# Kernel optimization log

Measured on AMD Instinct MI355X. Metric: run time of the kernel, lower is better.

Reference implementation:

```python
import jax, jax.numpy as jnp
import numpy as np

D_MODEL = 1024
NUM_HEADS = 16
HEAD_DIM = D_MODEL // NUM_HEADS


def setup_inputs() -> dict:
    key = jax.random.key(0)
    ks = jax.random.split(key, 5)
    scale = 1.0 / np.sqrt(D_MODEL)
    x = jax.random.normal(ks[0], (2, 2048, D_MODEL), dtype=jnp.float32)
    W_qkv = jax.random.normal(ks[1], (D_MODEL, 3 * D_MODEL), dtype=jnp.float32) * scale
    b_qkv = jnp.zeros((3 * D_MODEL,), dtype=jnp.float32)
    W_proj = jax.random.normal(ks[2], (D_MODEL, D_MODEL), dtype=jnp.float32) * scale
    b_proj = jnp.zeros((D_MODEL,), dtype=jnp.float32)
    return {"x": x, "W_qkv": W_qkv, "b_qkv": b_qkv, "W_proj": W_proj, "b_proj": b_proj}


def reference(x, W_qkv, b_qkv, W_proj, b_proj):
    B, S, D = x.shape
    qkv = x @ W_qkv + b_qkv                      # [B,S,3D]
    qkv = qkv.reshape(B, S, 3, NUM_HEADS, HEAD_DIM)
    qkv = jnp.transpose(qkv, (2, 0, 3, 1, 4))    # [3,B,H,S,hd]
    q, k, v = qkv[0], qkv[1], qkv[2]
    scores = jnp.einsum('bhqd,bhkd->bhqk', q, k) / jnp.sqrt(jnp.asarray(HEAD_DIM, x.dtype))
    probs = jax.nn.softmax(scores, axis=-1)
    out = jnp.einsum('bhqk,bhkd->bhqd', probs, v)  # [B,H,S,hd]
    out = jnp.transpose(out, (0, 2, 1, 3)).reshape(B, S, D)
    return out @ W_proj + b_proj
```

## Files before the change

### kernel.cpp

```cpp
#include <hip/hip_runtime.h>
#include <math.h>

#define B_ 2
#define S_ 2048
#define D_ 1024
#define H_ 16
#define HD_ 64

typedef __bf16 bf16x8 __attribute__((ext_vector_type(8)));
typedef __bf16 bf16x4 __attribute__((ext_vector_type(4)));
typedef __bf16 bf16x2 __attribute__((ext_vector_type(2)));
typedef float f32x4 __attribute__((ext_vector_type(4)));
typedef float f32x16 __attribute__((ext_vector_type(16)));
typedef unsigned u32x2 __attribute__((ext_vector_type(2)));

#define GLOAD16(gsrc, ldst) \
  __builtin_amdgcn_global_load_lds((const __attribute__((address_space(1))) void*)(gsrc), \
                                   (__attribute__((address_space(3))) void*)(ldst), 16, 0, 0)

#define QSCALE 0.18033688f

static __device__ __forceinline__ unsigned pack2(float a, float b) {
    bf16x2 v; v[0] = (__bf16)a; v[1] = (__bf16)b;
    return __builtin_bit_cast(unsigned, v);
}

__global__ __launch_bounds__(256) void prep_k(
    const float* __restrict__ x, __bf16* __restrict__ x_bf,
    const float* __restrict__ Wqkv, __bf16* __restrict__ wq_t,
    const float* __restrict__ Wproj, __bf16* __restrict__ wp_t)
{
    __shared__ float t[64][65];
    const int tid = threadIdx.x;
    const int bid = blockIdx.x;

    if (bid < 2048) {
        int i = (bid * 256 + tid) * 8;
        float4 a = *(const float4*)(x + i);
        float4 b = *(const float4*)(x + i + 4);
        bf16x8 v;
        v[0] = (__bf16)a.x; v[1] = (__bf16)a.y; v[2] = (__bf16)a.z; v[3] = (__bf16)a.w;
        v[4] = (__bf16)b.x; v[5] = (__bf16)b.y; v[6] = (__bf16)b.z; v[7] = (__bf16)b.w;
        *(bf16x8*)(x_bf + i) = v;
        return;
    }

    const float* in; __bf16* outp; int K, N, qcols; float qs; int bx, by;
    if (bid < 2816) {
        int tt = bid - 2048; bx = tt % 48; by = tt / 48;
        in = Wqkv; outp = wq_t; K = D_; N = 3 * D_; qcols = D_; qs = QSCALE;
    } else {
        int tt = bid - 2816; bx = tt % 16; by = tt / 16;
        in = Wproj; outp = wp_t; K = D_; N = D_; qcols = 0; qs = 1.0f;
    }
    const int bj = bx * 64;
    const int bi = by * 64;
    #pragma unroll
    for (int it = 0; it < 4; ++it) {
        int idx = (tid + it * 256) * 4;
        int r = idx >> 6, c = idx & 63;
        float4 v = *(const float4*)(in + (size_t)(bi + r) * N + bj + c);
        t[r][c] = v.x; t[r][c+1] = v.y; t[r][c+2] = v.z; t[r][c+3] = v.w;
    }
    __syncthreads();
    int j = tid & 63;
    int i0 = (tid >> 6) * 16;
    float s = (bj + j) < qcols ? qs : 1.0f;
    bf16x8 h0, h1;
    #pragma unroll
    for (int ii = 0; ii < 8; ++ii) h0[ii] = (__bf16)(t[i0 + ii][j] * s);
    #pragma unroll
    for (int ii = 0; ii < 8; ++ii) h1[ii] = (__bf16)(t[i0 + 8 + ii][j] * s);
    size_t o = (size_t)(bj + j) * K + bi + i0;
    *(bf16x8*)(outp + o) = h0; *(bf16x8*)(outp + o + 8) = h1;
}

__global__ __launch_bounds__(256) void gemm_nt_k(
    const __bf16* __restrict__ A, const __bf16* __restrict__ Bt,
    const float* __restrict__ bias, __bf16* __restrict__ C,
    int M, int N, int K, int qcols, float qs)
{
    constexpr int TSZ = 128 * 64;
    __shared__ __bf16 sA[TSZ];
    __shared__ __bf16 sB[TSZ];

    const int tid = threadIdx.x, w = tid >> 6, l = tid & 63;
    const int lr = l & 15, lg = l >> 4;
    const int bm = blockIdx.y * 128, bn = blockIdx.x * 128;
    const int wm = w >> 1, wn = w & 1;

    f32x4 acc[4][4] = {};

    for (int k0 = 0; k0 < K; k0 += 64) {
        __syncthreads();
        #pragma unroll
        for (int c = 0; c < 4; ++c) {
            int q = w * 4 + c;
            int r = q * 8 + (l >> 3);
            int sl = ((l & 7) ^ (r & 7)) * 8;
            GLOAD16(A + (size_t)(bm + r) * K + k0 + sl, sA + q * 512);
            GLOAD16(Bt + (size_t)(bn + r) * K + k0 + sl, sB + q * 512);
        }
        __syncthreads();
        #pragma unroll
        for (int kk = 0; kk < 2; ++kk) {
            bf16x8 ah[4], bh[4];
            #pragma unroll
            for (int i = 0; i < 4; ++i) {
                int ra = wm * 64 + i * 16 + lr;
                int sa = ((kk * 4 + lg) ^ (ra & 7)) * 8;
                ah[i] = *(const bf16x8*)(sA + ra * 64 + sa);
                int rb = wn * 64 + i * 16 + lr;
                int sb = ((kk * 4 + lg) ^ (rb & 7)) * 8;
                bh[i] = *(const bf16x8*)(sB + rb * 64 + sb);
            }
            #pragma unroll
            for (int mi = 0; mi < 4; ++mi)
                #pragma unroll
                for (int ni = 0; ni < 4; ++ni)
                    acc[mi][ni] = __builtin_amdgcn_mfma_f32_16x16x32_bf16(ah[mi], bh[ni], acc[mi][ni], 0, 0, 0);
        }
    }

    #pragma unroll
    for (int ni = 0; ni < 4; ++ni) {
        int col = bn + wn * 64 + ni * 16 + lr;
        float bv = bias[col];
        if (col < qcols) bv *= qs;
        #pragma unroll
        for (int mi = 0; mi < 4; ++mi) {
            #pragma unroll
            for (int r = 0; r < 4; ++r) {
                int row = bm + wm * 64 + mi * 16 + lg * 4 + r;
                float v = acc[mi][ni][r] + bv;
                C[(size_t)row * N + col] = (__bf16)v;
            }
        }
    }
}

__global__ __launch_bounds__(256) void gemm2_comb_k(
    const __bf16* __restrict__ P, const float* __restrict__ L,
    const __bf16* __restrict__ Bt, const float* __restrict__ bias,
    float* __restrict__ C)
{
    constexpr int K = D_, N = D_;
    constexpr size_t PS = (size_t)4096 * 1024;
    constexpr int LS = 4096 * 16;
    constexpr int TSZ = 128 * 64;
    __shared__ __bf16 sA[TSZ];
    __shared__ __bf16 sB[TSZ];

    const int tid = threadIdx.x, w = tid >> 6, l = tid & 63;
    const int lr = l & 15, lg = l >> 4;
    const int bm = blockIdx.y * 128, bn = blockIdx.x * 128;
    const int wm = w >> 1, wn = w & 1;

    int arow[4], asl[4];
    #pragma unroll
    for (int c = 0; c < 4; ++c) {
        int q = w * 4 + c;
        int r = q * 8 + (l >> 3);
        arow[c] = r;
        asl[c] = ((l & 7) ^ (r & 7)) * 8;
    }

    f32x4 acc[4][4] = {};

    for (int k0 = 0; k0 < K; k0 += 64) {
        const int h = k0 >> 6;
        __syncthreads();
        #pragma unroll
        for (int c = 0; c < 4; ++c) {
            int q = w * 4 + c;
            int sl = asl[c];
            GLOAD16(Bt + (size_t)(bn + arow[c]) * K + k0 + sl, sB + q * 512);
            size_t off = (size_t)(bm + arow[c]) * D_ + k0 + sl;
            bf16x8 p0 = *(const bf16x8*)(P + off);
            bf16x8 p1 = *(const bf16x8*)(P + PS + off);
            float inv = 1.0f / (L[(bm + arow[c]) * 16 + h] + L[LS + (bm + arow[c]) * 16 + h]);
            bf16x8 a;
            #pragma unroll
            for (int j = 0; j < 8; ++j)
                a[j] = (__bf16)(((float)p0[j] + (float)p1[j]) * inv);
            *(bf16x8*)(sA + q * 512 + l * 8) = a;
        }
        __syncthreads();
        #pragma unroll
        for (int kk = 0; kk < 2; ++kk) {
            bf16x8 ah[4], bh[4];
            #pragma unroll
            for (int i = 0; i < 4; ++i) {
                int ra = wm * 64 + i * 16 + lr;
                int sa = ((kk * 4 + lg) ^ (ra & 7)) * 8;
                ah[i] = *(const bf16x8*)(sA + ra * 64 + sa);
                int rb = wn * 64 + i * 16 + lr;
                int sb = ((kk * 4 + lg) ^ (rb & 7)) * 8;
                bh[i] = *(const bf16x8*)(sB + rb * 64 + sb);
            }
            #pragma unroll
            for (int mi = 0; mi < 4; ++mi)
                #pragma unroll
                for (int ni = 0; ni < 4; ++ni)
                    acc[mi][ni] = __builtin_amdgcn_mfma_f32_16x16x32_bf16(ah[mi], bh[ni], acc[mi][ni], 0, 0, 0);
        }
    }

    #pragma unroll
    for (int ni = 0; ni < 4; ++ni) {
        int col = bn + wn * 64 + ni * 16 + lr;
        float bv = bias[col];
        #pragma unroll
        for (int mi = 0; mi < 4; ++mi) {
            #pragma unroll
            for (int r = 0; r < 4; ++r) {
                int row = bm + wm * 64 + mi * 16 + lg * 4 + r;
                C[(size_t)row * N + col] = acc[mi][ni][r] + bv;
            }
        }
    }
}

__global__ __launch_bounds__(256, 2) void attn32_k(
    const __bf16* __restrict__ qkv, __bf16* __restrict__ Pout,
    float* __restrict__ Lout)
{
    __shared__ __bf16 Ks[2][64 * 64];
    __shared__ __bf16 Vt[2][64 * 64];

    const int tid = threadIdx.x, w = tid >> 6, l = tid & 63;
    const int q32 = l & 31, hi = l >> 5;
    const int bid = blockIdx.x;
    const int X = bid >> 5, hb = bid & 31;
    const int qt = X >> 1, kvh = X & 1;
    const int h = hb >> 1, b = hb & 1;
    const int q0 = qt * 256;
    const int kvbase = kvh * 1024;
    const size_t ldq = 3 * D_;
    const __bf16* Qg = qkv + (size_t)b * S_ * ldq + h * HD_;
    const __bf16* Kg = Qg + D_;
    const __bf16* Vg = Qg + 2 * D_;
    const int qg0 = q0 + w * 64 + q32;

    bf16x8 qf0[4], qf1[4];
    #pragma unroll
    for (int ds = 0; ds < 4; ++ds) {
        qf0[ds] = *(const bf16x8*)(Qg + (size_t)qg0 * ldq + ds * 16 + hi * 8);
        qf1[ds] = *(const bf16x8*)(Qg + (size_t)(qg0 + 32) * ldq + ds * 16 + hi * 8);
    }

    int krow[2], ksl[2], voff[2][8];
    const int vk = l;
    #pragma unroll
    for (int c = 0; c < 2; ++c) {
        int p = (w * 2 + c) * 64 + l;
        krow[c] = p >> 3;
        ksl[c]  = (p & 7) ^ (krow[c] & 7);
        int d0 = (w * 2 + c) * 8;
        #pragma unroll
        for (int j = 0; j < 8; ++j)
            voff[c][j] = (d0 + j) * 128 + (((vk >> 3) ^ j) * 16) + (vk & 7) * 2;
    }

    f32x16 o0[2] = {}, o1[2] = {};
    float lsum0 = 0.f, lsum1 = 0.f;
    bf16x8 vr[2];

    auto stageK = [&](int lt, int buf) {
        #pragma unroll
        for (int c = 0; c < 2; ++c)
            GLOAD16(Kg + (size_t)(kvbase + lt * 64 + krow[c]) * ldq + ksl[c] * 8,
                    &Ks[buf][(w * 2 + c) * 512]);
    };
    auto loadV = [&](int lt) {
        #pragma unroll
        for (int c = 0; c < 2; ++c)
            vr[c] = *(const bf16x8*)(Vg + (size_t)(kvbase + lt * 64 + vk) * ldq + (w * 2 + c) * 8);
    };
    auto writeV = [&](int buf) {
        #pragma unroll
        for (int c = 0; c < 2; ++c)
            #pragma unroll
            for (int j = 0; j < 8; ++j)
                *(__bf16*)((char*)&Vt[buf][0] + voff[c][j]) = vr[c][j];
    };

    auto smPack = [&](f32x16 sc[2], bf16x8 pa[2][2], float& ls) {
        float sum = 0.f;
        #pragma unroll
        for (int kb = 0; kb < 2; ++kb)
            #pragma unroll
            for (int i = 0; i < 16; ++i) {
                float pv = __builtin_amdgcn_exp2f(sc[kb][i]);
                sc[kb][i] = pv;
                sum += pv;
            }
        ls += sum;
        #pragma unroll
        for (int kb = 0; kb < 2; ++kb)
            #pragma unroll
            for (int tl = 0; tl < 2; ++tl) {
                int base = tl * 8;
                unsigned A0 = pack2(sc[kb][base + 0], sc[kb][base + 1]);
                unsigned A1 = pack2(sc[kb][base + 2], sc[kb][base + 3]);
                unsigned B0 = pack2(sc[kb][base + 4], sc[kb][base + 5]);
                unsigned B1 = pack2(sc[kb][base + 6], sc[kb][base + 7]);
                u32x2 s0 = __builtin_amdgcn_permlane32_swap(A0, B0, false, false);
                u32x2 s1 = __builtin_amdgcn_permlane32_swap(A1, B1, false, false);
                union { unsigned u[4]; bf16x8 v; } pu;
                pu.u[0] = s0[0]; pu.u[1] = s1[0]; pu.u[2] = s0[1]; pu.u[3] = s1[1];
                pa[kb][tl] = pu.v;
            }
    };

    auto computeTile = [&](int cur) {
        f32x16 sc0[2] = {}, sc1[2] = {};
        __builtin_amdgcn_s_setprio(1);
        #pragma unroll
        for (int kb = 0; kb < 2; ++kb) {
            int r = kb * 32 + q32;
            #pragma unroll
            for (int ds = 0; ds < 4; ++ds) {
                int slot = (ds * 2 + hi) ^ (r & 7);
                bf16x8 kf = *(const bf16x8*)((const char*)&Ks[cur][0] + r * 128 + slot * 16);
                sc0[kb] = __builtin_amdgcn_mfma_f32_32x32x16_bf16(kf, qf0[ds], sc0[kb], 0, 0, 0);
                sc1[kb] = __builtin_amdgcn_mfma_f32_32x32x16_bf16(kf, qf1[ds], sc1[kb], 0, 0, 0);
            }
        }
        __builtin_amdgcn_s_setprio(0);

        bf16x8 pa0[2][2], pa1[2][2];
        smPack(sc0, pa0, lsum0);
        smPack(sc1, pa1, lsum1);

        __builtin_amdgcn_s_setprio(1);
        #pragma unroll
        for (int db = 0; db < 2; ++db) {
            int dr = db * 32 + q32;
            #pragma unroll
            for (int tt = 0; tt < 4; ++tt) {
                int slot = (tt * 2 + hi) ^ (dr & 7);
                bf16x8 vf = *(const bf16x8*)((const char*)&Vt[cur][0] + dr * 128 + slot * 16);
                o0[db] = __builtin_amdgcn_mfma_f32_32x32x16_bf16(vf, pa0[tt >> 1][tt & 1], o0[db], 0, 0, 0);
                o1[db] = __builtin_amdgcn_mfma_f32_32x32x16_bf16(vf, pa1[tt >> 1][tt & 1], o1[db], 0, 0, 0);
            }
        }
        __builtin_amdgcn_s_setprio(0);
    };

    stageK(0, 0);
    loadV(0);
    writeV(0);
    __syncthreads();

    constexpr int NT = 16;
    for (int kt = 0; kt < NT; ++kt) {
        const int cur = kt & 1, nxt = cur ^ 1;
        if (kt < NT - 1) { stageK(kt + 1, nxt); loadV(kt + 1); }
        computeTile(cur);
        if (kt < NT - 1) writeV(nxt);
        __syncthreads();
    }

    lsum0 += __shfl_xor(lsum0, 32);
    lsum1 += __shfl_xor(lsum1, 32);
    const size_t orow0 = (size_t)b * S_ + qg0;
    __bf16* Pb0 = Pout + (size_t)kvh * (4096 * 1024) + orow0 * D_ + h * HD_;
    __bf16* Pb1 = Pb0 + (size_t)32 * D_;
    #pragma unroll
    for (int db = 0; db < 2; ++db)
        #pragma unroll
        for (int rg = 0; rg < 4; ++rg) {
            int d = db * 32 + 8 * rg + 4 * hi;
            bf16x4 ov0, ov1;
            #pragma unroll
            for (int i = 0; i < 4; ++i) {
                ov0[i] = (__bf16)o0[db][rg * 4 + i];
                ov1[i] = (__bf16)o1[db][rg * 4 + i];
            }
            *(bf16x4*)(Pb0 + d) = ov0;
            *(bf16x4*)(Pb1 + d) = ov1;
        }
    if (hi == 0) {
        Lout[(size_t)kvh * (4096 * 16) + orow0 * 16 + h] = lsum0;
        Lout[(size_t)kvh * (4096 * 16) + (orow0 + 32) * 16 + h] = lsum1;
    }
}

extern "C" void kernel_launch(void* const* d_in, const int* in_sizes, int n_in,
                              void* d_out, int out_size, void* d_ws, size_t ws_size,
                              hipStream_t stream) {
    const float* x     = (const float*)d_in[0];
    const float* Wqkv  = (const float*)d_in[1];
    const float* bqkv  = (const float*)d_in[2];
    const float* Wproj = (const float*)d_in[3];
    const float* bproj = (const float*)d_in[4];

    __bf16* ws = (__bf16*)d_ws;
    const size_t MB = 524288;
    __bf16* wp_t  = ws;
    __bf16* qkv   = ws + 2 * MB;
    __bf16* x_bf  = ws + 26 * MB;
    __bf16* wq_t  = ws + 34 * MB;
    __bf16* Pp    = ws + 34 * MB;
    float*  Lp    = (float*)(ws + 50 * MB);

    const int M = B_ * S_;

    prep_k<<<3072, 256, 0, stream>>>(x, x_bf, Wqkv, wq_t, Wproj, wp_t);

    gemm_nt_k<<<dim3(24, 32), 256, 0, stream>>>(
        x_bf, wq_t, bqkv, qkv, M, 3 * D_, D_, D_, QSCALE);

    attn32_k<<<512, 256, 0, stream>>>(qkv, Pp, Lp);

    gemm2_comb_k<<<dim3(8, 32), 256, 0, stream>>>(
        Pp, Lp, wp_t, bproj, (float*)d_out);
}
```

Before: 137.6 us.

## Double-buffer output GEMM, swizzle block order, stage QKV epilogue through LDS

The output-projection GEMM now double-buffers its LDS tiles and prefetches the next k-slice of partial attention outputs and weights while computing the current one. Both GEMMs remap a 1D grid with an XCD-style block swizzle to improve L2 locality. The QKV GEMM epilogue writes through shared memory so global stores become 16-byte coalesced vectors. The workspace layout also moves so the partial-output buffer overlaps x_bf instead of the transposed weights. The cost is doubled LDS use in gemm2 and more registers held for prefetched data.

```diff
diff --git a/kernel.cpp b/kernel.cpp
--- a/kernel.cpp
+++ b/kernel.cpp
@@ -81,12 +81,19 @@
     int M, int N, int K, int qcols, float qs)
 {
     constexpr int TSZ = 128 * 64;
-    __shared__ __bf16 sA[TSZ];
-    __shared__ __bf16 sB[TSZ];
+    __shared__ __bf16 smem[2 * TSZ];
+    __bf16* sA = smem;
+    __bf16* sB = smem + TSZ;
 
     const int tid = threadIdx.x, w = tid >> 6, l = tid & 63;
     const int lr = l & 15, lg = l >> 4;
-    const int bm = blockIdx.y * 128, bn = blockIdx.x * 128;
+
+    const int nwg = gridDim.x;
+    const int bidl = blockIdx.x;
+    const int swz = (bidl & 7) * (nwg >> 3) + (bidl >> 3);
+    const int nbx = N >> 7;
+    const int bx = swz % nbx, by = swz / nbx;
+    const int bm = by * 128, bn = bx * 128;
     const int wm = w >> 1, wn = w & 1;
 
     f32x4 acc[4][4] = {};
@@ -122,20 +129,28 @@
         }
     }
 
+    __syncthreads();
     #pragma unroll
     for (int ni = 0; ni < 4; ++ni) {
-        int col = bn + wn * 64 + ni * 16 + lr;
-        float bv = bias[col];
-        if (col < qcols) bv *= qs;
-        #pragma unroll
-        for (int mi = 0; mi < 4; ++mi) {
+        int col = wn * 64 + ni * 16 + lr;
+        float bv = bias[bn + col];
+        if (bn + col < qcols) bv *= qs;
+        #pragma unroll
+        for (int mi = 0; mi < 4; ++mi)
             #pragma unroll
             for (int r = 0; r < 4; ++r) {
-                int row = bm + wm * 64 + mi * 16 + lg * 4 + r;
-                float v = acc[mi][ni][r] + bv;
-                C[(size_t)row * N + col] = (__bf16)v;
-            }
-        }
+                int row = wm * 64 + mi * 16 + lg * 4 + r;
+                smem[row * 128 + col] = (__bf16)(acc[mi][ni][r] + bv);
+            }
+    }
+    __syncthreads();
+    #pragma unroll
+    for (int p = 0; p < 8; ++p) {
+        int idx = p * 2048 + tid * 8;
+        int row = idx >> 7;
+        int col = idx & 127;
+        bf16x8 v = *(const bf16x8*)(smem + idx);
+        *(bf16x8*)(C + (size_t)(bm + row) * N + bn + col) = v;
     }
 }
 
@@ -147,13 +162,18 @@
     constexpr int K = D_, N = D_;
     constexpr size_t PS = (size_t)4096 * 1024;
     constexpr int LS = 4096 * 16;
-    constexpr int TSZ = 128 * 64;
-    __shared__ __bf16 sA[TSZ];
-    __shared__ __bf16 sB[TSZ];
+    __shared__ __bf16 sA[2][128 * 64];
+    __shared__ __bf16 sB[2][128 * 64];
 
     const int tid = threadIdx.x, w = tid >> 6, l = tid & 63;
     const int lr = l & 15, lg = l >> 4;
-    const int bm = blockIdx.y * 128, bn = blockIdx.x * 128;
+
+    const int nwg = gridDim.x;
+    const int bidl = blockIdx.x;
+    const int swz = (bidl & 7) * (nwg >> 3) + (bidl >> 3);
+    const int nbx = N >> 7;
+    const int bx = swz % nbx, by = swz / nbx;
+    const int bm = by * 128, bn = bx * 128;
     const int wm = w >> 1, wn = w & 1;
 
     int arow[4], asl[4];
@@ -166,26 +186,46 @@
     }
 
     f32x4 acc[4][4] = {};
-
-    for (int k0 = 0; k0 < K; k0 += 64) {
+    bf16x8 p0r[4], p1r[4];
+    float invr[4];
+
+    auto issueA = [&](int k0) {
         const int h = k0 >> 6;
-        __syncthreads();
+        #pragma unroll
+        for (int c = 0; c < 4; ++c) {
+            size_t off = (size_t)(bm + arow[c]) * K + k0 + asl[c];
+            p0r[c] = *(const bf16x8*)(P + off);
+            p1r[c] = *(const bf16x8*)(P + PS + off);
+            invr[c] = 1.0f / (L[(bm + arow[c]) * 16 + h] + L[LS + (bm + arow[c]) * 16 + h]);
+        }
+    };
+    auto issueB = [&](int k0, int buf) {
         #pragma unroll
         for (int c = 0; c < 4; ++c) {
             int q = w * 4 + c;
-            int sl = asl[c];
-            GLOAD16(Bt + (size_t)(bn + arow[c]) * K + k0 + sl, sB + q * 512);
-            size_t off = (size_t)(bm + arow[c]) * D_ + k0 + sl;
-            bf16x8 p0 = *(const bf16x8*)(P + off);
-            bf16x8 p1 = *(const bf16x8*)(P + PS + off);
-            float inv = 1.0f / (L[(bm + arow[c]) * 16 + h] + L[LS + (bm + arow[c]) * 16 + h]);
+            GLOAD16(Bt + (size_t)(bn + arow[c]) * K + k0 + asl[c], &sB[buf][q * 512]);
+        }
+    };
+    auto writeA = [&](int buf) {
+        #pragma unroll
+        for (int c = 0; c < 4; ++c) {
+            int q = w * 4 + c;
             bf16x8 a;
             #pragma unroll
             for (int j = 0; j < 8; ++j)
-                a[j] = (__bf16)(((float)p0[j] + (float)p1[j]) * inv);
-            *(bf16x8*)(sA + q * 512 + l * 8) = a;
-        }
-        __syncthreads();
+                a[j] = (__bf16)(((float)p0r[c][j] + (float)p1r[c][j]) * invr[c]);
+            *(bf16x8*)(&sA[buf][q * 512 + l * 8]) = a;
+        }
+    };
+
+    issueA(0);
+    issueB(0, 0);
+    writeA(0);
+    __syncthreads();
+
+    for (int kt = 0; kt < 16; ++kt) {
+        const int cur = kt & 1, nxt = cur ^ 1;
+        if (kt < 15) { issueA((kt + 1) * 64); issueB((kt + 1) * 64, nxt); }
         #pragma unroll
         for (int kk = 0; kk < 2; ++kk) {
             bf16x8 ah[4], bh[4];
@@ -193,10 +233,10 @@
             for (int i = 0; i < 4; ++i) {
                 int ra = wm * 64 + i * 16 + lr;
                 int sa = ((kk * 4 + lg) ^ (ra & 7)) * 8;
-                ah[i] = *(const bf16x8*)(sA + ra * 64 + sa);
+                ah[i] = *(const bf16x8*)(&sA[cur][ra * 64 + sa]);
                 int rb = wn * 64 + i * 16 + lr;
                 int sb = ((kk * 4 + lg) ^ (rb & 7)) * 8;
-                bh[i] = *(const bf16x8*)(sB + rb * 64 + sb);
+                bh[i] = *(const bf16x8*)(&sB[cur][rb * 64 + sb]);
             }
             #pragma unroll
             for (int mi = 0; mi < 4; ++mi)
@@ -204,6 +244,8 @@
                 for (int ni = 0; ni < 4; ++ni)
                     acc[mi][ni] = __builtin_amdgcn_mfma_f32_16x16x32_bf16(ah[mi], bh[ni], acc[mi][ni], 0, 0, 0);
         }
+        if (kt < 15) writeA(nxt);
+        __syncthreads();
     }
 
     #pragma unroll
@@ -402,18 +444,18 @@
     __bf16* qkv   = ws + 2 * MB;
     __bf16* x_bf  = ws + 26 * MB;
     __bf16* wq_t  = ws + 34 * MB;
-    __bf16* Pp    = ws + 34 * MB;
-    float*  Lp    = (float*)(ws + 50 * MB);
+    __bf16* Pp    = ws + 26 * MB;
+    float*  Lp    = (float*)(ws + 42 * MB);
 
     const int M = B_ * S_;
 
     prep_k<<<3072, 256, 0, stream>>>(x, x_bf, Wqkv, wq_t, Wproj, wp_t);
 
-    gemm_nt_k<<<dim3(24, 32), 256, 0, stream>>>(
+    gemm_nt_k<<<768, 256, 0, stream>>>(
         x_bf, wq_t, bqkv, qkv, M, 3 * D_, D_, D_, QSCALE);
 
     attn32_k<<<512, 256, 0, stream>>>(qkv, Pp, Lp);
 
-    gemm2_comb_k<<<dim3(8, 32), 256, 0, stream>>>(
+    gemm2_comb_k<<<256, 256, 0, stream>>>(
         Pp, Lp, wp_t, bproj, (float*)d_out);
 }
```

Result: faster. 131.4 us (-4.5%).
